# Performance work log

Hardware: AMD Instinct MI355X
Metric: run time of the kernel (lower is better)

Reference implementation:

```python
import jax, jax.numpy as jnp
import numpy as np

EMBED = 1024
HEADS = 16
HEAD_DIM = EMBED // HEADS
FF = 4 * EMBED
B, S = 2, 2048
EPS = 1e-5


def layer_norm(x, g, b):
    mu = jnp.mean(x, axis=-1, keepdims=True)
    var = jnp.mean(jnp.square(x - mu), axis=-1, keepdims=True)
    return (x - mu) * jax.lax.rsqrt(var + EPS) * g + b


def setup_inputs() -> dict:
    key = jax.random.key(0)
    ks = jax.random.split(key, 12)
    sc = 0.02
    x = jax.random.normal(ks[0], (B, S, EMBED), dtype=jnp.float32)
    # causal mask: 1 where attending allowed (mask==0 -> -inf in original)
    mask = jnp.tril(jnp.ones((S, S), dtype=jnp.int32))[None, None]
    return {
        "x": x,
        "mask": mask,
        "ln1_g": jnp.ones((EMBED,), jnp.float32),
        "ln1_b": jnp.zeros((EMBED,), jnp.float32),
        "wq": sc * jax.random.normal(ks[1], (EMBED, EMBED), jnp.float32),
        "bq": jnp.zeros((EMBED,), jnp.float32),
        "wk": sc * jax.random.normal(ks[2], (EMBED, EMBED), jnp.float32),
        "bk": jnp.zeros((EMBED,), jnp.float32),
        "wv": sc * jax.random.normal(ks[3], (EMBED, EMBED), jnp.float32),
        "bv": jnp.zeros((EMBED,), jnp.float32),
        "wo": sc * jax.random.normal(ks[4], (EMBED, EMBED), jnp.float32),
        "bo": jnp.zeros((EMBED,), jnp.float32),
        "ln2_g": jnp.ones((EMBED,), jnp.float32),
        "ln2_b": jnp.zeros((EMBED,), jnp.float32),
        "w1": sc * jax.random.normal(ks[5], (EMBED, FF), jnp.float32),
        "b1": jnp.zeros((FF,), jnp.float32),
        "w2": sc * jax.random.normal(ks[6], (FF, EMBED), jnp.float32),
        "b2": jnp.zeros((EMBED,), jnp.float32),
    }


def reference(x, mask, ln1_g, ln1_b, wq, bq, wk, bk, wv, bv, wo, bo,
              ln2_g, ln2_b, w1, b1, w2, b2):
    bsz, seq, _ = x.shape
    residual = x
    h = layer_norm(x, ln1_g, ln1_b)
    # QKV projections -> [B, H, S, Dh]
    def split_heads(t):
        return t.reshape(bsz, seq, HEADS, HEAD_DIM).transpose(0, 2, 1, 3)
    q = split_heads(h @ wq + bq)
    k = split_heads(h @ wk + bk)
    v = split_heads(h @ wv + bv)
    scores = jnp.einsum('bhqd,bhkd->bhqk', q, k) / (HEAD_DIM ** 0.5)
    scores = jnp.where(mask == 0, -jnp.inf, scores)
    attn = jax.nn.softmax(scores, axis=-1)
    out = jnp.einsum('bhqk,bhkd->bhqd', attn, v)
    out = out.transpose(0, 2, 1, 3).reshape(bsz, seq, EMBED)
    out = out @ wo + bo
    x = residual + out
    residual = x
    h = layer_norm(x, ln2_g, ln2_b)
    h = jax.nn.gelu(h @ w1 + b1, approximate=False) @ w2 + b2
    return residual + h
```

## Files before the change

kernel.cpp:

```cpp
#include <hip/hip_runtime.h>

typedef unsigned short u16;
typedef unsigned int   u32;
typedef __attribute__((ext_vector_type(8))) short bf16x8;
typedef __attribute__((ext_vector_type(4))) float f32x4;

#define S_LEN 2048
#define EMB   1024
#define NH    16
#define HD    64
#define FF_DIM 4096
#define NROWS 4096

__device__ __forceinline__ float b2f(u16 u){ union{u32 i; float f;} c; c.i = ((u32)u)<<16; return c.f; }
__device__ __forceinline__ u16 f2b(float f){ union{float f; u32 u;} c; c.f=f; return (u16)((c.u + 0x8000u)>>16); }
__device__ __forceinline__ float gelu_f(float x){ return 0.5f*x*(1.0f + erff(x*0.70710678118f)); }

__device__ __forceinline__ void load_lds16(const u16* g, u16* l) {
    __builtin_amdgcn_global_load_lds((const __attribute__((address_space(1))) u32*)g,
                                     (__attribute__((address_space(3))) u32*)l, 16, 0, 0);
}

template<int XF32>
__global__ __launch_bounds__(256)
void ln_kernel(const void* __restrict__ Xv, const float* __restrict__ G,
               const float* __restrict__ Bv, u16* __restrict__ Y)
{
    const int row = blockIdx.x, t = threadIdx.x;
    float v0, v1, v2, v3;
    if constexpr (XF32) {
        float4 r4 = ((const float4*)((const float*)Xv + (size_t)row*EMB))[t];
        v0 = r4.x; v1 = r4.y; v2 = r4.z; v3 = r4.w;
    } else {
        const u16* xr = (const u16*)Xv + (size_t)row*EMB;
        uint2 raw = *(const uint2*)(xr + t*4);
        v0 = b2f(raw.x & 0xffff); v1 = b2f(raw.x >> 16);
        v2 = b2f(raw.y & 0xffff); v3 = b2f(raw.y >> 16);
    }
    float s  = v0+v1+v2+v3;
    float s2 = v0*v0+v1*v1+v2*v2+v3*v3;
    #pragma unroll
    for (int off = 1; off < 64; off <<= 1) {
        s  += __shfl_xor(s,  off, 64);
        s2 += __shfl_xor(s2, off, 64);
    }
    __shared__ float ps[4], ps2[4];
    const int w = t >> 6, lane = t & 63;
    if (lane == 0) { ps[w] = s; ps2[w] = s2; }
    __syncthreads();
    s  = ps[0]+ps[1]+ps[2]+ps[3];
    s2 = ps2[0]+ps2[1]+ps2[2]+ps2[3];
    const float mu   = s * (1.0f/EMB);
    const float rstd = rsqrtf(fmaxf(s2*(1.0f/EMB) - mu*mu, 0.f) + 1e-5f);
    float4 g4 = ((const float4*)G)[t];
    float4 c4 = ((const float4*)Bv)[t];
    u32 lo = (u32)f2b((v0-mu)*rstd*g4.x + c4.x) | ((u32)f2b((v1-mu)*rstd*g4.y + c4.y) << 16);
    u32 hi = (u32)f2b((v2-mu)*rstd*g4.z + c4.z) | ((u32)f2b((v3-mu)*rstd*g4.w + c4.w) << 16);
    uint2 o; o.x = lo; o.y = hi;
    *(uint2*)(Y + (size_t)row*EMB + t*4) = o;
}

__global__ __launch_bounds__(256)
void transpose_k(const float* __restrict__ in, u16* __restrict__ out, int K, int N)
{
    __shared__ __align__(16) u16 T[64*72];
    const int k0 = blockIdx.y*64, n0 = blockIdx.x*64, t = threadIdx.x;
    #pragma unroll
    for (int c = 0; c < 4; ++c) {
        int e = t*4 + c*1024, ki = e >> 6, nj = e & 63;
        float4 f = *(const float4*)(in + (size_t)(k0+ki)*N + n0 + nj);
        ushort4 s4; s4.x = f2b(f.x); s4.y = f2b(f.y); s4.z = f2b(f.z); s4.w = f2b(f.w);
        *(ushort4*)&T[ki*72 + nj] = s4;
    }
    __syncthreads();
    #pragma unroll
    for (int c = 0; c < 2; ++c) {
        int e = t*8 + c*2048, ni = e >> 6, kj = e & 63;
        uint4 v; u16* pv = (u16*)&v;
        #pragma unroll
        for (int j = 0; j < 8; ++j) pv[j] = T[(kj+j)*72 + ni];
        *(uint4*)(out + (size_t)(n0+ni)*K + k0 + kj) = v;
    }
}

__global__ __launch_bounds__(256)
void vtrans(const u16* __restrict__ in, u16* __restrict__ out)
{
    __shared__ __align__(16) u16 T[64*72];
    const int bh = blockIdx.y, s0 = blockIdx.x*64, t = threadIdx.x;
    const size_t base = (size_t)bh * (S_LEN*HD);
    #pragma unroll
    for (int c = 0; c < 2; ++c) {
        int e = t*8 + c*2048, r = e >> 6, d = e & 63;
        *(uint4*)&T[r*72 + d] = *(const uint4*)(in + base + (size_t)(s0 + r)*HD + d);
    }
    __syncthreads();
    #pragma unroll
    for (int c = 0; c < 2; ++c) {
        int e = t*8 + c*2048, d = e >> 6, sj = e & 63;
        uint4 v; u16* pv = (u16*)&v;
        #pragma unroll
        for (int j = 0; j < 8; ++j) pv[j] = T[(sj + j)*72 + d];
        *(uint4*)(out + base + (size_t)d*S_LEN + s0 + sj) = v;
    }
}

template<int MODE, int RESF, int OUTF, int TM>
__global__ __launch_bounds__(256)
void gemm_bt(const u16* __restrict__ A, const u16* __restrict__ Bt,
             const float* __restrict__ bias, const float* __restrict__ bias2,
             const float* __restrict__ bias3, const void* __restrict__ res,
             void* __restrict__ C, void* __restrict__ C2, void* __restrict__ C3,
             int M, int N, int K)
{
    constexpr int MT  = (TM == 128) ? 4 : 2;
    constexpr int ACH = TM * 32;
    __shared__ __align__(16) u16 Sm[(TM == 128) ? 16384 : 12288];
    u16* As = Sm;
    u16* Bs = Sm + 2*ACH;
    const int t = threadIdx.x;
    const int m0 = (TM == 128) ? blockIdx.y*128 : blockIdx.x*64;
    const int n0 = (TM == 128) ? blockIdx.x*128 : blockIdx.y*128;
    const int wave = t >> 6, lane = t & 63;
    const int wm = (wave >> 1) * (TM/2);
    const int wn = (wave & 1) * 64;
    const int lr = lane & 15, quad = lane >> 4;

    const u16* gA = A  + (size_t)(m0 + wave*16 + (lane >> 2))*K + (lane & 3)*8;
    const u16* gB = Bt + (size_t)(n0 + wave*16 + (lane >> 2))*K + (lane & 3)*8;
    u16* lA = As + wave*512;
    u16* lB = Bs + wave*512;

    f32x4 acc[MT][4];
    const f32x4 fzero = {0.f, 0.f, 0.f, 0.f};
    #pragma unroll
    for (int mt = 0; mt < MT; ++mt)
        #pragma unroll
        for (int nt = 0; nt < 4; ++nt) acc[mt][nt] = fzero;

    for (int kt = 0; kt < K; kt += 64) {
        __syncthreads();
        #pragma unroll
        for (int c = 0; c < 2; ++c) {
            load_lds16(gA + c*32, lA + c*ACH);
            if constexpr (TM == 128)
                load_lds16(gA + (size_t)64*K + c*32, lA + c*ACH + 2048);
            load_lds16(gB + c*32, lB + c*4096);
            load_lds16(gB + (size_t)64*K + c*32, lB + c*4096 + 2048);
        }
        gA += 64; gB += 64;
        __syncthreads();
        #pragma unroll
        for (int ks = 0; ks < 2; ++ks) {
            bf16x8 af[MT], bf[4];
            #pragma unroll
            for (int i = 0; i < MT; ++i)
                af[i] = *(const bf16x8*)&As[ks*ACH + (wm + i*16 + lr)*32 + quad*8];
            #pragma unroll
            for (int i = 0; i < 4; ++i)
                bf[i] = *(const bf16x8*)&Bs[ks*4096 + (wn + i*16 + lr)*32 + quad*8];
            #pragma unroll
            for (int mt = 0; mt < MT; ++mt)
                #pragma unroll
                for (int nt = 0; nt < 4; ++nt)
                    acc[mt][nt] = __builtin_amdgcn_mfma_f32_16x16x32_bf16(af[mt], bf[nt], acc[mt][nt], 0, 0, 0);
        }
    }

    u16* qkvDst = nullptr;
    if constexpr (MODE == 5) {
        int seg = n0 >> 10;
        qkvDst = (u16*)(seg == 0 ? C : (seg == 1 ? C2 : C3));
    }

    #pragma unroll
    for (int c = 0; c < (TM == 128 ? 2 : 1); ++c) {
        __syncthreads();
        if (TM == 64 || (wave >> 1) == c) {
            #pragma unroll
            for (int nt = 0; nt < 4; ++nt) {
                int colL = wn + nt*16 + lr;
                float bval;
                if constexpr (MODE == 5) {
                    int col = n0 + colL;
                    int seg = col >> 10, cs = col & 1023;
                    bval = (seg == 0 ? bias : (seg == 1 ? bias2 : bias3))[cs];
                } else {
                    bval = bias[n0 + colL];
                }
                #pragma unroll
                for (int mt = 0; mt < MT; ++mt) {
                    #pragma unroll
                    for (int r = 0; r < 4; ++r) {
                        int rowL = (TM == 128 ? mt*16 : wm + mt*16) + quad*4 + r;
                        float v = acc[mt][nt][r] + bval;
                        if constexpr (MODE == 2) v = gelu_f(v);
                        Sm[rowL*136 + colL] = f2b(v);
                    }
                }
            }
        }
        __syncthreads();
        #pragma unroll
        for (int i = 0; i < 4; ++i) {
            const int rowL = wave*16 + i*4 + (lane >> 4);
            const int colL = (lane & 15)*8;
            const int row  = m0 + c*64 + rowL;
            const u16* src = &Sm[rowL*136 + colL];
            if constexpr (MODE == 5) {
                int cs = (n0 + colL) & 1023;
                int h = cs >> 6, d = cs & 63;
                int b_ = row >> 11, s = row & 2047;
                u16* dst = qkvDst + ((((size_t)(b_*NH + h))*S_LEN + s) << 6) + d;
                *(uint4*)dst = *(const uint4*)src;
            } else {
                size_t base = (size_t)row*N + n0 + colL;
                if constexpr (MODE == 1 || OUTF) {
                    uint4 sv = *(const uint4*)src;
                    const u16* sp = (const u16*)&sv;
                    float f[8];
                    #pragma unroll
                    for (int j = 0; j < 8; ++j) f[j] = b2f(sp[j]);
                    if constexpr (MODE == 1) {
                        if constexpr (RESF) {
                            const float* rp = (const float*)res + base;
                            float4 r0 = *(const float4*)rp, r1 = *(const float4*)(rp+4);
                            f[0]+=r0.x; f[1]+=r0.y; f[2]+=r0.z; f[3]+=r0.w;
                            f[4]+=r1.x; f[5]+=r1.y; f[6]+=r1.z; f[7]+=r1.w;
                        } else {
                            uint4 rv = *(const uint4*)((const u16*)res + base);
                            const u16* rp = (const u16*)&rv;
                            #pragma unroll
                            for (int j = 0; j < 8; ++j) f[j] += b2f(rp[j]);
                        }
                    }
                    if constexpr (OUTF) {
                        float* op = (float*)C + base;
                        float4 o0 = {f[0],f[1],f[2],f[3]}, o1 = {f[4],f[5],f[6],f[7]};
                        *(float4*)op = o0; *(float4*)(op+4) = o1;
                    } else {
                        u16 ov[8];
                        #pragma unroll
                        for (int j = 0; j < 8; ++j) ov[j] = f2b(f[j]);
                        *(uint4*)((u16*)C + base) = *(const uint4*)ov;
                    }
                } else {
                    *(uint4*)((u16*)C + base) = *(const uint4*)src;
                }
            }
        }
    }
}

__global__ __launch_bounds__(256, 2)
void attn_kernel(const u16* __restrict__ Q, const u16* __restrict__ Kg,
                 const u16* __restrict__ Vt, u16* __restrict__ O)
{
    const int bh = blockIdx.x;
    const int pr = blockIdx.y;
    const int qta = pr, qtb = 31 - pr;
    const int t = threadIdx.x, wave = t >> 6, lane = t & 63;
    const int lr = lane & 15, quad = lane >> 4;

    __shared__ __align__(16) u16 Ks[4096];
    __shared__ __align__(16) u16 Vs[4096];
    __shared__ __align__(16) u16 Ps[4][16*72];

    const size_t qkbase = (size_t)bh * (S_LEN*HD);
    const int b = bh >> 4, h = bh & 15;
    u16* Pw = Ps[wave];
    const f32x4 fzero = {0.f, 0.f, 0.f, 0.f};

    const u16* qpa = Q + qkbase + (size_t)(qta*64 + wave*16 + lr)*HD + quad*8;
    const u16* qpb = Q + qkbase + (size_t)(qtb*64 + wave*16 + lr)*HD + quad*8;
    bf16x8 qa0 = *(const bf16x8*)qpa, qa1 = *(const bf16x8*)(qpa + 32);
    bf16x8 qb0 = *(const bf16x8*)qpb, qb1 = *(const bf16x8*)(qpb + 32);

    f32x4 oa[4], ob[4];
    float la[4], lb[4];
    #pragma unroll
    for (int dt = 0; dt < 4; ++dt) { oa[dt] = fzero; ob[dt] = fzero; }
    #pragma unroll
    for (int r = 0; r < 4; ++r) { la[r] = 0.f; lb[r] = 0.f; }

    const u16* gK = Kg + qkbase + (size_t)(wave*16 + (lane>>2))*HD + (lane&3)*8;
    const u16* gV = Vt + qkbase + (size_t)(wave*16 + (lane>>2))*S_LEN + (lane&3)*8;
    u16* lK = Ks + wave*512;
    u16* lV = Vs + wave*512;

    const int qrow_qa = qta*64 + wave*16 + quad*4;
    const int qrow_qb = qtb*64 + wave*16 + quad*4;

    for (int kb = 0; kb <= qtb; ++kb) {
        __syncthreads();
        load_lds16(gK + (size_t)kb*4096,      lK);
        load_lds16(gK + (size_t)kb*4096 + 32, lK + 2048);
        load_lds16(gV + kb*64,                lV);
        load_lds16(gV + kb*64 + 32,           lV + 2048);
        __syncthreads();

        #pragma unroll
        for (int tile = 0; tile < 2; ++tile) {
            const int qt = tile ? qta : qtb;
            if (tile && kb > qta) break;
            bf16x8 qf0 = tile ? qa0 : qb0;
            bf16x8 qf1 = tile ? qa1 : qb1;
            f32x4* oacc = tile ? oa : ob;
            float* lp   = tile ? la : lb;
            const int qrowq = tile ? qrow_qa : qrow_qb;

            f32x4 sc[4];
            #pragma unroll
            for (int kt2 = 0; kt2 < 4; ++kt2) {
                bf16x8 kf0 = *(const bf16x8*)&Ks[(kt2*16 + lr)*32 + quad*8];
                bf16x8 kf1 = *(const bf16x8*)&Ks[2048 + (kt2*16 + lr)*32 + quad*8];
                sc[kt2] = __builtin_amdgcn_mfma_f32_16x16x32_bf16(qf0, kf0, fzero, 0, 0, 0);
                sc[kt2] = __builtin_amdgcn_mfma_f32_16x16x32_bf16(qf1, kf1, sc[kt2], 0, 0, 0);
            }
            const bool diag = (kb == qt);
            #pragma unroll
            for (int r = 0; r < 4; ++r) {
                #pragma unroll
                for (int kt2 = 0; kt2 < 4; ++kt2) {
                    int kcol = kb*64 + kt2*16 + lr;
                    float p = (!diag || kcol <= qrowq + r) ? __expf(fminf(sc[kt2][r]*0.125f, 30.f)) : 0.f;
                    lp[r] += p;
                    Pw[(quad*4 + r)*72 + kt2*16 + lr] = f2b(p);
                }
            }
            bf16x8 pf0 = *(const bf16x8*)&Pw[lr*72 + quad*8];
            bf16x8 pf1 = *(const bf16x8*)&Pw[lr*72 + 32 + quad*8];
            #pragma unroll
            for (int dt = 0; dt < 4; ++dt) {
                bf16x8 vf0 = *(const bf16x8*)&Vs[(dt*16 + lr)*32 + quad*8];
                bf16x8 vf1 = *(const bf16x8*)&Vs[2048 + (dt*16 + lr)*32 + quad*8];
                oacc[dt] = __builtin_amdgcn_mfma_f32_16x16x32_bf16(pf0, vf0, oacc[dt], 0, 0, 0);
                oacc[dt] = __builtin_amdgcn_mfma_f32_16x16x32_bf16(pf1, vf1, oacc[dt], 0, 0, 0);
            }
        }
    }

    #pragma unroll
    for (int tile = 0; tile < 2; ++tile) {
        const int qt = tile ? qta : qtb;
        f32x4* oacc = tile ? oa : ob;
        float* lp   = tile ? la : lb;
        #pragma unroll
        for (int r = 0; r < 4; ++r) {
            float v = lp[r];
            v += __shfl_xor(v, 1, 64); v += __shfl_xor(v, 2, 64);
            v += __shfl_xor(v, 4, 64); v += __shfl_xor(v, 8, 64);
            lp[r] = 1.0f / fmaxf(v, 1e-20f);
        }
        #pragma unroll
        for (int dt = 0; dt < 4; ++dt)
            #pragma unroll
            for (int r = 0; r < 4; ++r)
                Pw[(quad*4 + r)*64 + dt*16 + lr] = f2b(oacc[dt][r] * lp[r]);

        const int q = lane >> 2, d0 = (lane & 3)*16;
        u16* dst = O + ((size_t)(b*S_LEN + qt*64 + wave*16 + q))*EMB + h*HD + d0;
        *(uint4*)(dst)     = *(uint4*)&Pw[q*64 + d0];
        *(uint4*)(dst + 8) = *(uint4*)&Pw[q*64 + d0 + 8];
    }
}

extern "C" void kernel_launch(void* const* d_in, const int* in_sizes, int n_in,
                              void* d_out, int out_size, void* d_ws, size_t ws_size,
                              hipStream_t stream)
{
    (void)in_sizes; (void)n_in; (void)out_size; (void)ws_size;
    const float* x    = (const float*)d_in[0];
    const float* ln1g = (const float*)d_in[2];
    const float* ln1b = (const float*)d_in[3];
    const float* wq = (const float*)d_in[4];  const float* bq = (const float*)d_in[5];
    const float* wk = (const float*)d_in[6];  const float* bk = (const float*)d_in[7];
    const float* wv = (const float*)d_in[8];  const float* bv = (const float*)d_in[9];
    const float* wo = (const float*)d_in[10]; const float* bo = (const float*)d_in[11];
    const float* ln2g = (const float*)d_in[12]; const float* ln2b = (const float*)d_in[13];
    const float* w1 = (const float*)d_in[14]; const float* b1 = (const float*)d_in[15];
    const float* w2 = (const float*)d_in[16]; const float* b2 = (const float*)d_in[17];

    u16* ws = (u16*)d_ws;
    const size_t M1 = 1u << 20;
    u16* wqkvT = ws + 0*M1;
    u16* wqT = ws + 0*M1;
    u16* wkT = ws + 1*M1;
    u16* wvT = ws + 2*M1;
    u16* woT = ws + 3*M1;
    u16* w2T = ws + 0*M1;
    u16* w1T = ws + 4*M1;
    u16* h0  = ws + 8*M1;
    u16* qb  = ws + 12*M1;
    u16* kb  = ws + 16*M1;
    u16* vT  = ws + 20*M1;
    u16* ao  = ws + 24*M1;
    u16* vb  = ws + 24*M1;
    u16* x1  = ws + 28*M1;
    u16* fb  = ws + 12*M1;

    dim3 blk(256);
    transpose_k<<<dim3(16,16), blk, 0, stream>>>(wq, wqT, EMB, EMB);
    transpose_k<<<dim3(16,16), blk, 0, stream>>>(wk, wkT, EMB, EMB);
    transpose_k<<<dim3(16,16), blk, 0, stream>>>(wv, wvT, EMB, EMB);
    transpose_k<<<dim3(16,16), blk, 0, stream>>>(wo, woT, EMB, EMB);
    transpose_k<<<dim3(64,16), blk, 0, stream>>>(w1, w1T, EMB, FF_DIM);

    ln_kernel<1><<<NROWS, blk, 0, stream>>>(x, ln1g, ln1b, h0);

    gemm_bt<5,0,0,128><<<dim3(24,32), blk, 0, stream>>>(h0, wqkvT, bq, bk, bv, nullptr,
                                                        qb, kb, vb, NROWS, 3072, EMB);

    vtrans<<<dim3(32,32), blk, 0, stream>>>(vb, vT);

    attn_kernel<<<dim3(32,16), blk, 0, stream>>>(qb, kb, vT, ao);

    gemm_bt<1,1,0,64><<<dim3(64,8), blk, 0, stream>>>(ao, woT, bo, nullptr, nullptr, x,
                                                      x1, nullptr, nullptr, NROWS, EMB, EMB);

    transpose_k<<<dim3(16,64), blk, 0, stream>>>(w2, w2T, FF_DIM, EMB);

    ln_kernel<0><<<NROWS, blk, 0, stream>>>(x1, ln2g, ln2b, h0);

    gemm_bt<2,0,0,128><<<dim3(32,32), blk, 0, stream>>>(h0, w1T, b1, nullptr, nullptr, nullptr,
                                                        fb, nullptr, nullptr, NROWS, FF_DIM, EMB);
    gemm_bt<1,0,1,64><<<dim3(64,8), blk, 0, stream>>>(fb, w2T, b2, nullptr, nullptr, x1,
                                                      d_out, nullptr, nullptr, NROWS, EMB, FF_DIM);
}
```

Baseline: 415.2 us.

## Double-buffer LDS tiles in GEMM and attention kernels to overlap loads with MFMA

The GEMM main loop now works on 32-wide K chunks with two LDS buffers. The next chunk's global-to-LDS load is issued before computing the current one, and only one barrier is used per chunk. The attention kernel likewise double-buffers its K/V tiles, prefetching the next key block while computing the current one. This aims to hide global load latency behind matrix math, at the cost of doubled K/V LDS in attention (possible occupancy loss) and more barriers per unit of K in the GEMM.

```diff
diff --git a/kernel.cpp b/kernel.cpp
--- a/kernel.cpp
+++ b/kernel.cpp
@@ -128,8 +128,6 @@
 
     const u16* gA = A  + (size_t)(m0 + wave*16 + (lane >> 2))*K + (lane & 3)*8;
     const u16* gB = Bt + (size_t)(n0 + wave*16 + (lane >> 2))*K + (lane & 3)*8;
-    u16* lA = As + wave*512;
-    u16* lB = Bs + wave*512;
 
     f32x4 acc[MT][4];
     const f32x4 fzero = {0.f, 0.f, 0.f, 0.f};
@@ -138,34 +136,40 @@
         #pragma unroll
         for (int nt = 0; nt < 4; ++nt) acc[mt][nt] = fzero;
 
-    for (int kt = 0; kt < K; kt += 64) {
+    auto STAGE = [&](int cc, int p) {
+        const u16* a = gA + cc*32;
+        const u16* b = gB + cc*32;
+        load_lds16(a, As + p*ACH + wave*512);
+        if constexpr (TM == 128)
+            load_lds16(a + (size_t)64*K, As + p*ACH + wave*512 + 2048);
+        load_lds16(b, Bs + p*4096 + wave*512);
+        load_lds16(b + (size_t)64*K, Bs + p*4096 + wave*512 + 2048);
+    };
+    auto COMPUTE = [&](int p) {
+        bf16x8 af[MT], bf[4];
+        #pragma unroll
+        for (int i = 0; i < MT; ++i)
+            af[i] = *(const bf16x8*)&As[p*ACH + (wm + i*16 + lr)*32 + quad*8];
+        #pragma unroll
+        for (int i = 0; i < 4; ++i)
+            bf[i] = *(const bf16x8*)&Bs[p*4096 + (wn + i*16 + lr)*32 + quad*8];
+        #pragma unroll
+        for (int mt = 0; mt < MT; ++mt)
+            #pragma unroll
+            for (int nt = 0; nt < 4; ++nt)
+                acc[mt][nt] = __builtin_amdgcn_mfma_f32_16x16x32_bf16(af[mt], bf[nt], acc[mt][nt], 0, 0, 0);
+    };
+
+    const int NC = K >> 5;
+    STAGE(0, 0);
+    __syncthreads();
+    for (int c = 0; c < NC - 1; ++c) {
+        const int p = c & 1;
+        STAGE(c + 1, p ^ 1);
+        COMPUTE(p);
         __syncthreads();
-        #pragma unroll
-        for (int c = 0; c < 2; ++c) {
-            load_lds16(gA + c*32, lA + c*ACH);
-            if constexpr (TM == 128)
-                load_lds16(gA + (size_t)64*K + c*32, lA + c*ACH + 2048);
-            load_lds16(gB + c*32, lB + c*4096);
-            load_lds16(gB + (size_t)64*K + c*32, lB + c*4096 + 2048);
-        }
-        gA += 64; gB += 64;
-        __syncthreads();
-        #pragma unroll
-        for (int ks = 0; ks < 2; ++ks) {
-            bf16x8 af[MT], bf[4];
-            #pragma unroll
-            for (int i = 0; i < MT; ++i)
-                af[i] = *(const bf16x8*)&As[ks*ACH + (wm + i*16 + lr)*32 + quad*8];
-            #pragma unroll
-            for (int i = 0; i < 4; ++i)
-                bf[i] = *(const bf16x8*)&Bs[ks*4096 + (wn + i*16 + lr)*32 + quad*8];
-            #pragma unroll
-            for (int mt = 0; mt < MT; ++mt)
-                #pragma unroll
-                for (int nt = 0; nt < 4; ++nt)
-                    acc[mt][nt] = __builtin_amdgcn_mfma_f32_16x16x32_bf16(af[mt], bf[nt], acc[mt][nt], 0, 0, 0);
-        }
-    }
+    }
+    COMPUTE((NC - 1) & 1);
 
     u16* qkvDst = nullptr;
     if constexpr (MODE == 5) {
@@ -262,8 +266,8 @@
     const int t = threadIdx.x, wave = t >> 6, lane = t & 63;
     const int lr = lane & 15, quad = lane >> 4;
 
-    __shared__ __align__(16) u16 Ks[4096];
-    __shared__ __align__(16) u16 Vs[4096];
+    __shared__ __align__(16) u16 Ks[8192];
+    __shared__ __align__(16) u16 Vs[8192];
     __shared__ __align__(16) u16 Ps[4][16*72];
 
     const size_t qkbase = (size_t)bh * (S_LEN*HD);
@@ -285,19 +289,22 @@
 
     const u16* gK = Kg + qkbase + (size_t)(wave*16 + (lane>>2))*HD + (lane&3)*8;
     const u16* gV = Vt + qkbase + (size_t)(wave*16 + (lane>>2))*S_LEN + (lane&3)*8;
-    u16* lK = Ks + wave*512;
-    u16* lV = Vs + wave*512;
 
     const int qrow_qa = qta*64 + wave*16 + quad*4;
     const int qrow_qb = qtb*64 + wave*16 + quad*4;
 
+    auto STAGEKV = [&](int kb, int p) {
+        load_lds16(gK + (size_t)kb*4096,      Ks + p*4096 + wave*512);
+        load_lds16(gK + (size_t)kb*4096 + 32, Ks + p*4096 + wave*512 + 2048);
+        load_lds16(gV + kb*64,                Vs + p*4096 + wave*512);
+        load_lds16(gV + kb*64 + 32,           Vs + p*4096 + wave*512 + 2048);
+    };
+
+    STAGEKV(0, 0);
+    __syncthreads();
     for (int kb = 0; kb <= qtb; ++kb) {
-        __syncthreads();
-        load_lds16(gK + (size_t)kb*4096,      lK);
-        load_lds16(gK + (size_t)kb*4096 + 32, lK + 2048);
-        load_lds16(gV + kb*64,                lV);
-        load_lds16(gV + kb*64 + 32,           lV + 2048);
-        __syncthreads();
+        const int p = kb & 1;
+        if (kb < qtb) STAGEKV(kb + 1, p ^ 1);
 
         #pragma unroll
         for (int tile = 0; tile < 2; ++tile) {
@@ -312,8 +319,8 @@
             f32x4 sc[4];
             #pragma unroll
             for (int kt2 = 0; kt2 < 4; ++kt2) {
-                bf16x8 kf0 = *(const bf16x8*)&Ks[(kt2*16 + lr)*32 + quad*8];
-                bf16x8 kf1 = *(const bf16x8*)&Ks[2048 + (kt2*16 + lr)*32 + quad*8];
+                bf16x8 kf0 = *(const bf16x8*)&Ks[p*4096 + (kt2*16 + lr)*32 + quad*8];
+                bf16x8 kf1 = *(const bf16x8*)&Ks[p*4096 + 2048 + (kt2*16 + lr)*32 + quad*8];
                 sc[kt2] = __builtin_amdgcn_mfma_f32_16x16x32_bf16(qf0, kf0, fzero, 0, 0, 0);
                 sc[kt2] = __builtin_amdgcn_mfma_f32_16x16x32_bf16(qf1, kf1, sc[kt2], 0, 0, 0);
             }
@@ -323,21 +330,22 @@
                 #pragma unroll
                 for (int kt2 = 0; kt2 < 4; ++kt2) {
                     int kcol = kb*64 + kt2*16 + lr;
-                    float p = (!diag || kcol <= qrowq + r) ? __expf(fminf(sc[kt2][r]*0.125f, 30.f)) : 0.f;
-                    lp[r] += p;
-                    Pw[(quad*4 + r)*72 + kt2*16 + lr] = f2b(p);
+                    float pv = (!diag || kcol <= qrowq + r) ? __expf(fminf(sc[kt2][r]*0.125f, 30.f)) : 0.f;
+                    lp[r] += pv;
+                    Pw[(quad*4 + r)*72 + kt2*16 + lr] = f2b(pv);
                 }
             }
             bf16x8 pf0 = *(const bf16x8*)&Pw[lr*72 + quad*8];
             bf16x8 pf1 = *(const bf16x8*)&Pw[lr*72 + 32 + quad*8];
             #pragma unroll
             for (int dt = 0; dt < 4; ++dt) {
-                bf16x8 vf0 = *(const bf16x8*)&Vs[(dt*16 + lr)*32 + quad*8];
-                bf16x8 vf1 = *(const bf16x8*)&Vs[2048 + (dt*16 + lr)*32 + quad*8];
+                bf16x8 vf0 = *(const bf16x8*)&Vs[p*4096 + (dt*16 + lr)*32 + quad*8];
+                bf16x8 vf1 = *(const bf16x8*)&Vs[p*4096 + 2048 + (dt*16 + lr)*32 + quad*8];
                 oacc[dt] = __builtin_amdgcn_mfma_f32_16x16x32_bf16(pf0, vf0, oacc[dt], 0, 0, 0);
                 oacc[dt] = __builtin_amdgcn_mfma_f32_16x16x32_bf16(pf1, vf1, oacc[dt], 0, 0, 0);
             }
         }
+        __syncthreads();
     }
 
     #pragma unroll
```

Measured after the change: 419.8 us. No clear change (+1.1%).

## Add 256x256-tile 8-wave pipelined GEMM for QKV and FFN1 projections

Applied to the files above, without the earlier changes.

Introduces a new bf16 MFMA GEMM kernel with 256x256 output tiles, 512 threads, swizzled LDS and a 4-stage half-K double-buffered pipeline. Global-to-LDS loads are interleaved with MFMA phases under explicit vmcnt waits and priority hints. It replaces the 128-tile GEMM for the fused QKV projection and the FFN up-projection to raise data reuse and overlap loads with compute. It also swaps erff in GELU for a polynomial approximation (Abramowitz-Stegun) using a fast exp, which trades exactness for cheaper epilogue math. Grids become small (192 and 256 blocks), which may underfill the GPU's CUs.

```diff
diff --git a/kernel.cpp b/kernel.cpp
--- a/kernel.cpp
+++ b/kernel.cpp
@@ -14,7 +14,16 @@
 
 __device__ __forceinline__ float b2f(u16 u){ union{u32 i; float f;} c; c.i = ((u32)u)<<16; return c.f; }
 __device__ __forceinline__ u16 f2b(float f){ union{float f; u32 u;} c; c.f=f; return (u16)((c.u + 0x8000u)>>16); }
-__device__ __forceinline__ float gelu_f(float x){ return 0.5f*x*(1.0f + erff(x*0.70710678118f)); }
+__device__ __forceinline__ float gelu_f(float x){
+    float z  = x * 0.70710678118f;
+    float az = fabsf(z);
+    float t  = 1.0f / (1.0f + 0.3275911f * az);
+    float p  = ((((1.061405429f*t - 1.453152027f)*t + 1.421413741f)*t - 0.284496736f)*t + 0.254829592f)*t;
+    float e  = __expf(-az*az);
+    float erfv = 1.0f - p*e;
+    erfv = (z < 0.f) ? -erfv : erfv;
+    return 0.5f*x*(1.0f + erfv);
+}
 
 __device__ __forceinline__ void load_lds16(const u16* g, u16* l) {
     __builtin_amdgcn_global_load_lds((const __attribute__((address_space(1))) u32*)g,
@@ -102,6 +111,152 @@
         #pragma unroll
         for (int j = 0; j < 8; ++j) pv[j] = T[(sj + j)*72 + d];
         *(uint4*)(out + base + (size_t)d*S_LEN + s0 + sj) = v;
+    }
+}
+
+__device__ __forceinline__ void stage2(const u16* s0, const u16* s1, int koff, u16* dst, int wave){
+    load_lds16(s0 + koff, dst + wave*512);
+    load_lds16(s1 + koff, dst + 4096 + wave*512);
+}
+
+template<int CBUF, int KS, int NHH, int TAILVM>
+__device__ __forceinline__ void phase256(u16* Ls, f32x4 (&acc)[8][4],
+    int wm, int wn, int lr, int quad, int wave,
+    const u16* s0, const u16* s1, int koff, u16* dst)
+{
+    const u16* ak = Ls + CBUF*32768 + KS*8192;
+    const u16* bk = Ls + CBUF*32768 + 16384 + KS*8192;
+    bf16x8 af[8], bf[2];
+    #pragma unroll
+    for (int mf = 0; mf < 8; ++mf) {
+        int off = (wm*128 + mf*16 + lr)*32 + quad*8;
+        af[mf] = *(const bf16x8*)(ak + (off ^ ((off>>3)&0x18)));
+    }
+    #pragma unroll
+    for (int nf = 0; nf < 2; ++nf) {
+        int off = (wn*64 + NHH*32 + nf*16 + lr)*32 + quad*8;
+        bf[nf] = *(const bf16x8*)(bk + (off ^ ((off>>3)&0x18)));
+    }
+    stage2(s0, s1, koff, dst, wave);
+    __builtin_amdgcn_s_barrier();
+    __builtin_amdgcn_s_setprio(1);
+    #pragma unroll
+    for (int mf = 0; mf < 8; ++mf) {
+        acc[mf][NHH*2+0] = __builtin_amdgcn_mfma_f32_16x16x32_bf16(af[mf], bf[0], acc[mf][NHH*2+0], 0, 0, 0);
+        acc[mf][NHH*2+1] = __builtin_amdgcn_mfma_f32_16x16x32_bf16(af[mf], bf[1], acc[mf][NHH*2+1], 0, 0, 0);
+    }
+    __builtin_amdgcn_s_setprio(0);
+    if constexpr (TAILVM) asm volatile("s_waitcnt vmcnt(8)" ::: "memory");
+    __builtin_amdgcn_s_barrier();
+}
+
+template<int MODE>
+__global__ __launch_bounds__(512, 2)
+void gemm256(const u16* __restrict__ A, const u16* __restrict__ Bt,
+             const float* __restrict__ bias, const float* __restrict__ bias2,
+             const float* __restrict__ bias3,
+             void* __restrict__ C, void* __restrict__ C2, void* __restrict__ C3,
+             int M, int N, int K)
+{
+    (void)M;
+    __shared__ __align__(16) u16 Ls[65536];
+    const int t = threadIdx.x;
+    const int wave = t >> 6, lane = t & 63;
+    const int wm = wave >> 2, wn = wave & 3;
+    const int lr = lane & 15, quad = lane >> 4;
+    const int n0 = blockIdx.x*256, m0 = blockIdx.y*256;
+
+    const int c0 = wave*64 + lane, c1 = 512 + wave*64 + lane;
+    const int l0 = c0 ^ ((c0 >> 3) & 3), l1 = c1 ^ ((c1 >> 3) & 3);
+    const int r0 = l0 >> 2, g0 = l0 & 3;
+    const int r1 = l1 >> 2, g1 = l1 & 3;
+    const u16* srcA0 = A  + (size_t)(m0 + r0)*K + g0*8;
+    const u16* srcA1 = A  + (size_t)(m0 + r1)*K + g1*8;
+    const u16* srcB0 = Bt + (size_t)(n0 + r0)*K + g0*8;
+    const u16* srcB1 = Bt + (size_t)(n0 + r1)*K + g1*8;
+
+    u16* A00 = Ls + 0;
+    u16* A01 = Ls + 8192;
+    u16* B00 = Ls + 16384;
+    u16* B01 = Ls + 16384 + 8192;
+    u16* A10 = Ls + 32768;
+    u16* A11 = Ls + 32768 + 8192;
+    u16* B10 = Ls + 32768 + 16384;
+    u16* B11 = Ls + 32768 + 16384 + 8192;
+
+    f32x4 acc[8][4];
+    const f32x4 fzero = {0.f, 0.f, 0.f, 0.f};
+    #pragma unroll
+    for (int i = 0; i < 8; ++i)
+        #pragma unroll
+        for (int j = 0; j < 4; ++j) acc[i][j] = fzero;
+
+    const int NT = K >> 6;
+
+    stage2(srcA0, srcA1, 0,   A00, wave);
+    stage2(srcB0, srcB1, 0,   B00, wave);
+    stage2(srcA0, srcA1, 32,  A01, wave);
+    stage2(srcB0, srcB1, 32,  B01, wave);
+    stage2(srcA0, srcA1, 64,  A10, wave);
+    stage2(srcB0, srcB1, 64,  B10, wave);
+    asm volatile("s_waitcnt vmcnt(8)" ::: "memory");
+    __builtin_amdgcn_s_barrier();
+
+    for (int U = 0; U < NT; U += 2) {
+        const int k1 = ((U+1) & (NT-1))*64;
+        const int k2 = ((U+2) & (NT-1))*64;
+        const int k3 = ((U+3) & (NT-1))*64;
+        phase256<0,0,0,0>(Ls, acc, wm, wn, lr, quad, wave, srcA0, srcA1, k1+32, A11);
+        phase256<0,0,1,1>(Ls, acc, wm, wn, lr, quad, wave, srcB0, srcB1, k1+32, B11);
+        phase256<0,1,0,0>(Ls, acc, wm, wn, lr, quad, wave, srcA0, srcA1, k2,    A00);
+        phase256<0,1,1,1>(Ls, acc, wm, wn, lr, quad, wave, srcB0, srcB1, k2,    B00);
+        phase256<1,0,0,0>(Ls, acc, wm, wn, lr, quad, wave, srcA0, srcA1, k2+32, A01);
+        phase256<1,0,1,1>(Ls, acc, wm, wn, lr, quad, wave, srcB0, srcB1, k2+32, B01);
+        phase256<1,1,0,0>(Ls, acc, wm, wn, lr, quad, wave, srcA0, srcA1, k3,    A10);
+        phase256<1,1,1,1>(Ls, acc, wm, wn, lr, quad, wave, srcB0, srcB1, k3,    B10);
+    }
+
+    asm volatile("s_waitcnt vmcnt(0)" ::: "memory");
+    __syncthreads();
+
+    float bv[4];
+    #pragma unroll
+    for (int nf = 0; nf < 4; ++nf) {
+        const int col = n0 + wn*64 + nf*16 + lr;
+        if constexpr (MODE == 5) {
+            const int seg = n0 >> 10;
+            bv[nf] = (seg == 0 ? bias : (seg == 1 ? bias2 : bias3))[col & 1023];
+        } else {
+            bv[nf] = bias[col];
+        }
+    }
+    #pragma unroll
+    for (int mf = 0; mf < 8; ++mf)
+        #pragma unroll
+        for (int nf = 0; nf < 4; ++nf)
+            #pragma unroll
+            for (int r = 0; r < 4; ++r) {
+                float v = acc[mf][nf][r] + bv[nf];
+                if constexpr (MODE == 2) v = gelu_f(v);
+                Ls[(wm*128 + mf*16 + quad*4 + r)*256 + wn*64 + nf*16 + lr] = f2b(v);
+            }
+    __syncthreads();
+    #pragma unroll
+    for (int j = 0; j < 16; ++j) {
+        const int idx = j*512 + t;
+        const int rr = idx >> 5, ck = idx & 31;
+        const u16* src = Ls + rr*256 + ck*8;
+        const int row = m0 + rr, col = n0 + ck*8;
+        if constexpr (MODE == 5) {
+            const int seg = n0 >> 10;
+            u16* dstb = (u16*)(seg == 0 ? C : (seg == 1 ? C2 : C3));
+            const int cs = col & 1023;
+            const int h = cs >> 6, d = cs & 63;
+            const int b_ = row >> 11, s = row & 2047;
+            *(uint4*)(dstb + ((((size_t)(b_*NH + h))*S_LEN + s) << 6) + d) = *(const uint4*)src;
+        } else {
+            *(uint4*)((u16*)C + (size_t)row*N + col) = *(const uint4*)src;
+        }
     }
 }
 
@@ -408,8 +563,8 @@
 
     ln_kernel<1><<<NROWS, blk, 0, stream>>>(x, ln1g, ln1b, h0);
 
-    gemm_bt<5,0,0,128><<<dim3(24,32), blk, 0, stream>>>(h0, wqkvT, bq, bk, bv, nullptr,
-                                                        qb, kb, vb, NROWS, 3072, EMB);
+    gemm256<5><<<dim3(12,16), dim3(512), 0, stream>>>(h0, wqkvT, bq, bk, bv,
+                                                      qb, kb, vb, NROWS, 3072, EMB);
 
     vtrans<<<dim3(32,32), blk, 0, stream>>>(vb, vT);
 
@@ -422,8 +577,9 @@
 
     ln_kernel<0><<<NROWS, blk, 0, stream>>>(x1, ln2g, ln2b, h0);
 
-    gemm_bt<2,0,0,128><<<dim3(32,32), blk, 0, stream>>>(h0, w1T, b1, nullptr, nullptr, nullptr,
-                                                        fb, nullptr, nullptr, NROWS, FF_DIM, EMB);
+    gemm256<2><<<dim3(16,16), dim3(512), 0, stream>>>(h0, w1T, b1, nullptr, nullptr,
+                                                      fb, nullptr, nullptr, NROWS, FF_DIM, EMB);
+
     gemm_bt<1,0,1,64><<<dim3(64,8), blk, 0, stream>>>(fb, w2T, b2, nullptr, nullptr, x1,
                                                       d_out, nullptr, nullptr, NROWS, EMB, FF_DIM);
 }
```

Measured after the change: 374.6 us. 9.8% less time.
